# Performance work log

Hardware: AMD Instinct MI355X
Metric: run time of the kernel (lower is better)

Reference implementation:

```python
import jax, jax.numpy as jnp
import numpy as np

DT = 0.1  # integration step used by LiquidCell.forward default

def setup_inputs() -> dict:
    key = jax.random.key(0)
    k1, k2, k3 = jax.random.split(key, 3)
    B, T, I, H = 32, 1024, 512, 1024
    x = jax.random.normal(k1, (B, T, I), dtype=jnp.float32)
    # Linear weights stored torch-style: [out_features, in_features]
    W = jax.random.normal(k2, (H, I), dtype=jnp.float32) * 0.02
    U = jax.random.normal(k3, (H, H), dtype=jnp.float32) * 0.02
    b = jnp.zeros((H,), dtype=jnp.float32)
    tau = jnp.ones((H,), dtype=jnp.float32)
    return {"x": x, "W": W, "U": U, "b": b, "tau": tau}

def reference(x, W, U, b, tau):
    # x: [B, T, I]; returns (h_final [B, H], all_states [B, T, H])
    B = x.shape[0]
    H = tau.shape[0]
    # Precompute input projections for all timesteps in one big GEMM: [B, T, H]
    xW = jnp.einsum('bti,hi->bth', x, W)
    inv_tau = 1.0 / tau

    def step(h, xW_t):
        # xW_t: [B, H]
        act = jnp.tanh(xW_t + h @ U.T + b)
        h_new = h + DT * (-inv_tau * h + act)
        return h_new, h_new

    h0 = jnp.zeros((B, H), dtype=x.dtype)
    xs = jnp.swapaxes(xW, 0, 1)  # [T, B, H]
    h_final, states = jax.lax.scan(step, h0, xs)
    all_states = jnp.swapaxes(states, 0, 1)  # [B, T, H]
    return h_final, all_states
```

## Files before the change

### kernel.cpp

```cpp
#include <hip/hip_runtime.h>


#define DT 0.1f
#define BB 32
#define TT 1024
#define II 512
#define HH 1024

typedef __attribute__((ext_vector_type(4))) float f32x4;
typedef __attribute__((ext_vector_type(8))) short s16x8;

__device__ __forceinline__ unsigned short f2bf(float f) {
  unsigned int u = __builtin_bit_cast(unsigned int, f);
  u += 0x7fffu + ((u >> 16) & 1u);
  return (unsigned short)(u >> 16);
}

__global__ __launch_bounds__(256) void cvt_u_kernel(const float* __restrict__ U,
                                                    unsigned short* __restrict__ Ub) {
  int i4 = (blockIdx.x * 256 + threadIdx.x) * 4;
  float4 v = *(const float4*)(U + i4);
  ushort4 o;
  o.x = f2bf(v.x); o.y = f2bf(v.y); o.z = f2bf(v.z); o.w = f2bf(v.w);
  *(ushort4*)(Ub + i4) = o;
}

#define P1_LDK 36

__global__ __launch_bounds__(256) void xw_gemm(const float* __restrict__ x,
                                               const float* __restrict__ W,
                                               float* __restrict__ out) {
  __shared__ __align__(16) float Xs[128 * P1_LDK];
  __shared__ __align__(16) float Ws_s[128 * P1_LDK];
  const int tid = threadIdx.x;
  const int m0 = blockIdx.y * 128;
  const int n0 = blockIdx.x * 128;
  const int ty = tid >> 4;
  const int tx = tid & 15;
  const int lrow = tid >> 3;
  const int lf = tid & 7;

  float acc[8][8];
#pragma unroll
  for (int i = 0; i < 8; ++i)
#pragma unroll
    for (int j = 0; j < 8; ++j) acc[i][j] = 0.0f;

  for (int kk = 0; kk < II; kk += 32) {
#pragma unroll
    for (int p = 0; p < 4; ++p) {
      int r = lrow + 32 * p;
      float4 vx = *(const float4*)&x[(m0 + r) * II + kk + 4 * lf];
      *(float4*)&Xs[r * P1_LDK + 4 * lf] = vx;
      float4 vw = *(const float4*)&W[(n0 + r) * II + kk + 4 * lf];
      *(float4*)&Ws_s[r * P1_LDK + 4 * lf] = vw;
    }
    __syncthreads();
#pragma unroll
    for (int kq = 0; kq < 32; kq += 4) {
      float4 a[8], b[8];
#pragma unroll
      for (int i = 0; i < 4; ++i) {
        a[i]     = *(const float4*)&Xs[(ty * 4 + i) * P1_LDK + kq];
        a[i + 4] = *(const float4*)&Xs[(ty * 4 + i + 64) * P1_LDK + kq];
      }
#pragma unroll
      for (int j = 0; j < 8; ++j)
        b[j] = *(const float4*)&Ws_s[(tx + 16 * j) * P1_LDK + kq];
#pragma unroll
      for (int i = 0; i < 8; ++i)
#pragma unroll
        for (int j = 0; j < 8; ++j) {
          acc[i][j] += a[i].x * b[j].x;
          acc[i][j] += a[i].y * b[j].y;
          acc[i][j] += a[i].z * b[j].z;
          acc[i][j] += a[i].w * b[j].w;
        }
    }
    __syncthreads();
  }
#pragma unroll
  for (int i = 0; i < 8; ++i) {
    int m = m0 + ty * 4 + (i < 4 ? i : 64 + i - 4);
#pragma unroll
    for (int j = 0; j < 8; ++j)
      out[m * HH + n0 + tx + 16 * j] = acc[i][j];
  }
}

#define LDH 1032

__global__ __launch_bounds__(64) void liquid_step(
    const unsigned short* __restrict__ hb,
    const unsigned short* __restrict__ Ub,
    float* __restrict__ hf,
    unsigned short* __restrict__ hb_out,
    float* __restrict__ states,
    const float* __restrict__ bias,
    const float* __restrict__ tau,
    int t) {
  __shared__ __align__(16) unsigned short h_s[16 * LDH];
  __shared__ __align__(16) unsigned short u_s[8 * LDH];

  const int l = threadIdx.x;
  const int bid = blockIdx.x;
  const int mg = bid >> 7;
  const int jg = bid & 127;
  const int n = l & 15;
  const int q = l >> 4;
  const int jloc = n & 7;
  const int j = jg * 8 + jloc;

  float xw[4], hold[4];
#pragma unroll
  for (int r = 0; r < 4; ++r) {
    int b = mg * 16 + q * 4 + r;
    xw[r] = states[(b * TT + t) * HH + j];
    hold[r] = hf[b * HH + j];
  }
  float bj = bias[j];
  float invt = 1.0f / tau[j];

#pragma unroll
  for (int r = 0; r < 16; ++r) {
    int b = mg * 16 + r;
#pragma unroll
    for (int hh = 0; hh < 2; ++hh) {
      uint4 v = *(const uint4*)(hb + b * HH + hh * 512 + l * 8);
      *(uint4*)&h_s[r * LDH + hh * 512 + l * 8] = v;
    }
  }
#pragma unroll
  for (int r = 0; r < 8; ++r) {
    int jr = jg * 8 + r;
#pragma unroll
    for (int hh = 0; hh < 2; ++hh) {
      uint4 v = *(const uint4*)(Ub + jr * HH + hh * 512 + l * 8);
      *(uint4*)&u_s[r * LDH + hh * 512 + l * 8] = v;
    }
  }
  __syncthreads();

  f32x4 acc0 = {0.f, 0.f, 0.f, 0.f}, acc1 = {0.f, 0.f, 0.f, 0.f};
  const int ar = n;
  const int br = jloc;
  const int ko = q * 8;
#pragma unroll
  for (int kc = 0; kc < 32; kc += 2) {
    s16x8 a0 = *(const s16x8*)&h_s[ar * LDH + kc * 32 + ko];
    s16x8 b0 = *(const s16x8*)&u_s[br * LDH + kc * 32 + ko];
    acc0 = __builtin_amdgcn_mfma_f32_16x16x32_bf16(a0, b0, acc0, 0, 0, 0);
    s16x8 a1 = *(const s16x8*)&h_s[ar * LDH + (kc + 1) * 32 + ko];
    s16x8 b1 = *(const s16x8*)&u_s[br * LDH + (kc + 1) * 32 + ko];
    acc1 = __builtin_amdgcn_mfma_f32_16x16x32_bf16(a1, b1, acc1, 0, 0, 0);
  }
  f32x4 acc = acc0 + acc1;

#pragma unroll
  for (int r = 0; r < 4; ++r) {
    float pre = xw[r] + acc[r] + bj;
    float act = tanhf(pre);
    float hnew = hold[r] + DT * (act - invt * hold[r]);
    if (n < 8) {
      int b = mg * 16 + q * 4 + r;
      hf[b * HH + j] = hnew;
      hb_out[b * HH + j] = f2bf(hnew);
      states[(b * TT + t) * HH + j] = hnew;
    }
  }
}

extern "C" void kernel_launch(void* const* d_in, const int* in_sizes, int n_in,
                              void* d_out, int out_size, void* d_ws, size_t ws_size,
                              hipStream_t stream) {
  const float* x    = (const float*)d_in[0];
  const float* W    = (const float*)d_in[1];
  const float* U    = (const float*)d_in[2];
  const float* bias = (const float*)d_in[3];
  const float* tau  = (const float*)d_in[4];

  float* out = (float*)d_out;
  float* hf = out;
  float* states = out + BB * HH;

  unsigned short* Ub = (unsigned short*)d_ws;
  unsigned short* hb = Ub + (size_t)HH * HH;

  hipMemsetAsync(hf, 0, BB * HH * sizeof(float), stream);
  hipMemsetAsync(hb, 0, BB * HH * sizeof(unsigned short), stream);

  cvt_u_kernel<<<(HH * HH) / (256 * 4), 256, 0, stream>>>(U, Ub);

  xw_gemm<<<dim3(HH / 128, (BB * TT) / 128), 256, 0, stream>>>(x, W, states);

  for (int t = 0; t < TT; ++t) {
    liquid_step<<<256, 64, 0, stream>>>(hb, Ub, hf, hb, states, bias, tau, t);
  }
}
```

Measured before the change: 5.041 ms.

## Replace per-timestep launches with a persistent scan kernel using flag-based sync

Replaces the 1024 separate per-step kernel launches with one persistent kernel of 128 single-wave workgroups. Each workgroup keeps its slice of U in registers and loops over all timesteps. Workgroups in the same batch group synchronise through agent-scope atomic flags, and the bf16 hidden state is double-buffered. This removes per-launch overhead and the repeated reload of U, and it prefetches the next step's xW. It relies on all 128 workgroups being co-resident for the spin-wait to make progress, and it adds polling latency on every step.

```diff
diff --git a/kernel.cpp b/kernel.cpp
--- a/kernel.cpp
+++ b/kernel.cpp
@@ -88,86 +88,94 @@
   }
 }
 
-#define LDH 1032
-
-__global__ __launch_bounds__(64) void liquid_step(
-    const unsigned short* __restrict__ hb,
+__global__ __launch_bounds__(64, 1) void liquid_scan(
     const unsigned short* __restrict__ Ub,
+    unsigned short* __restrict__ hbuf,
+    int* flags,
     float* __restrict__ hf,
-    unsigned short* __restrict__ hb_out,
     float* __restrict__ states,
     const float* __restrict__ bias,
-    const float* __restrict__ tau,
-    int t) {
-  __shared__ __align__(16) unsigned short h_s[16 * LDH];
-  __shared__ __align__(16) unsigned short u_s[8 * LDH];
-
+    const float* __restrict__ tau) {
   const int l = threadIdx.x;
-  const int bid = blockIdx.x;
-  const int mg = bid >> 7;
-  const int jg = bid & 127;
+  const int wg = blockIdx.x;
+  const int mg = wg >> 6;
+  const int jg = wg & 63;
   const int n = l & 15;
   const int q = l >> 4;
-  const int jloc = n & 7;
-  const int j = jg * 8 + jloc;
-
-  float xw[4], hold[4];
-#pragma unroll
-  for (int r = 0; r < 4; ++r) {
-    int b = mg * 16 + q * 4 + r;
-    xw[r] = states[(b * TT + t) * HH + j];
-    hold[r] = hf[b * HH + j];
+  const int j = jg * 16 + n;
+  const int arow = mg * 16 + n;
+
+  s16x8 ufrag[32];
+#pragma unroll
+  for (int kc = 0; kc < 32; ++kc)
+    ufrag[kc] = *(const s16x8*)(Ub + (size_t)j * HH + kc * 32 + q * 8);
+
+  const float bj = bias[j];
+  const float invt = 1.0f / tau[j];
+  int* const myflags = flags + mg * 64;
+
+  float hold[4] = {0.f, 0.f, 0.f, 0.f};
+  float xw[4];
+#pragma unroll
+  for (int r = 0; r < 4; ++r)
+    xw[r] = states[((size_t)(mg * 16 + q * 4 + r) * TT + 0) * HH + j];
+
+  for (int t = 0; t < TT; ++t) {
+    const unsigned short* hin = hbuf + (size_t)(t & 1) * (BB * HH);
+    unsigned short* hout = hbuf + (size_t)((t + 1) & 1) * (BB * HH);
+
+    if (t > 0) {
+      for (;;) {
+        int f = __hip_atomic_load(&myflags[l], __ATOMIC_RELAXED,
+                                  __HIP_MEMORY_SCOPE_AGENT);
+        if (__all(f >= t)) break;
+      }
+      __builtin_amdgcn_fence(__ATOMIC_ACQUIRE, "agent");
+    }
+
+    s16x8 af[32];
+#pragma unroll
+    for (int kc = 0; kc < 32; ++kc)
+      af[kc] = *(const s16x8*)(hin + (size_t)arow * HH + kc * 32 + q * 8);
+
+    const int tn = (t + 1 < TT) ? t + 1 : TT - 1;
+    float xwn[4];
+#pragma unroll
+    for (int r = 0; r < 4; ++r)
+      xwn[r] = states[((size_t)(mg * 16 + q * 4 + r) * TT + tn) * HH + j];
+
+    f32x4 a0 = {0.f, 0.f, 0.f, 0.f}, a1 = {0.f, 0.f, 0.f, 0.f};
+    f32x4 a2 = {0.f, 0.f, 0.f, 0.f}, a3 = {0.f, 0.f, 0.f, 0.f};
+#pragma unroll
+    for (int kc = 0; kc < 32; kc += 4) {
+      a0 = __builtin_amdgcn_mfma_f32_16x16x32_bf16(af[kc + 0], ufrag[kc + 0], a0, 0, 0, 0);
+      a1 = __builtin_amdgcn_mfma_f32_16x16x32_bf16(af[kc + 1], ufrag[kc + 1], a1, 0, 0, 0);
+      a2 = __builtin_amdgcn_mfma_f32_16x16x32_bf16(af[kc + 2], ufrag[kc + 2], a2, 0, 0, 0);
+      a3 = __builtin_amdgcn_mfma_f32_16x16x32_bf16(af[kc + 3], ufrag[kc + 3], a3, 0, 0, 0);
+    }
+    f32x4 acc = (a0 + a1) + (a2 + a3);
+
+#pragma unroll
+    for (int r = 0; r < 4; ++r) {
+      const int b = mg * 16 + q * 4 + r;
+      float pre = xw[r] + acc[r] + bj;
+      float act = tanhf(pre);
+      float hnew = hold[r] + DT * (act - invt * hold[r]);
+      hold[r] = hnew;
+      states[((size_t)b * TT + t) * HH + j] = hnew;
+      hout[b * HH + j] = f2bf(hnew);
+      xw[r] = xwn[r];
+    }
+
+    __builtin_amdgcn_fence(__ATOMIC_RELEASE, "agent");
+    if (l == 0)
+      __hip_atomic_store(&myflags[jg], t + 1, __ATOMIC_RELAXED,
+                         __HIP_MEMORY_SCOPE_AGENT);
   }
-  float bj = bias[j];
-  float invt = 1.0f / tau[j];
-
-#pragma unroll
-  for (int r = 0; r < 16; ++r) {
-    int b = mg * 16 + r;
-#pragma unroll
-    for (int hh = 0; hh < 2; ++hh) {
-      uint4 v = *(const uint4*)(hb + b * HH + hh * 512 + l * 8);
-      *(uint4*)&h_s[r * LDH + hh * 512 + l * 8] = v;
-    }
-  }
-#pragma unroll
-  for (int r = 0; r < 8; ++r) {
-    int jr = jg * 8 + r;
-#pragma unroll
-    for (int hh = 0; hh < 2; ++hh) {
-      uint4 v = *(const uint4*)(Ub + jr * HH + hh * 512 + l * 8);
-      *(uint4*)&u_s[r * LDH + hh * 512 + l * 8] = v;
-    }
-  }
-  __syncthreads();
-
-  f32x4 acc0 = {0.f, 0.f, 0.f, 0.f}, acc1 = {0.f, 0.f, 0.f, 0.f};
-  const int ar = n;
-  const int br = jloc;
-  const int ko = q * 8;
-#pragma unroll
-  for (int kc = 0; kc < 32; kc += 2) {
-    s16x8 a0 = *(const s16x8*)&h_s[ar * LDH + kc * 32 + ko];
-    s16x8 b0 = *(const s16x8*)&u_s[br * LDH + kc * 32 + ko];
-    acc0 = __builtin_amdgcn_mfma_f32_16x16x32_bf16(a0, b0, acc0, 0, 0, 0);
-    s16x8 a1 = *(const s16x8*)&h_s[ar * LDH + (kc + 1) * 32 + ko];
-    s16x8 b1 = *(const s16x8*)&u_s[br * LDH + (kc + 1) * 32 + ko];
-    acc1 = __builtin_amdgcn_mfma_f32_16x16x32_bf16(a1, b1, acc1, 0, 0, 0);
-  }
-  f32x4 acc = acc0 + acc1;
-
-#pragma unroll
-  for (int r = 0; r < 4; ++r) {
-    float pre = xw[r] + acc[r] + bj;
-    float act = tanhf(pre);
-    float hnew = hold[r] + DT * (act - invt * hold[r]);
-    if (n < 8) {
-      int b = mg * 16 + q * 4 + r;
-      hf[b * HH + j] = hnew;
-      hb_out[b * HH + j] = f2bf(hnew);
-      states[(b * TT + t) * HH + j] = hnew;
-    }
-  }
+
+#pragma unroll
+  for (int r = 0; r < 4; ++r)
+    hf[(mg * 16 + q * 4 + r) * HH + j] = hold[r];
 }
 
 extern "C" void kernel_launch(void* const* d_in, const int* in_sizes, int n_in,
@@ -184,16 +192,16 @@
   float* states = out + BB * HH;
 
   unsigned short* Ub = (unsigned short*)d_ws;
-  unsigned short* hb = Ub + (size_t)HH * HH;
-
-  hipMemsetAsync(hf, 0, BB * HH * sizeof(float), stream);
-  hipMemsetAsync(hb, 0, BB * HH * sizeof(unsigned short), stream);
+  unsigned short* hbuf = Ub + (size_t)HH * HH;
+  int* flags = (int*)(hbuf + 2 * BB * HH);
+
+  hipMemsetAsync(hbuf, 0,
+                 2 * BB * HH * sizeof(unsigned short) + 128 * sizeof(int),
+                 stream);
 
   cvt_u_kernel<<<(HH * HH) / (256 * 4), 256, 0, stream>>>(U, Ub);
 
   xw_gemm<<<dim3(HH / 128, (BB * TT) / 128), 256, 0, stream>>>(x, W, states);
 
-  for (int t = 0; t < TT; ++t) {
-    liquid_step<<<256, 64, 0, stream>>>(hb, Ub, hf, hb, states, bias, tau, t);
-  }
-}
+  liquid_scan<<<128, 64, 0, stream>>>(Ub, hbuf, flags, hf, states, bias, tau);
+}
```

New measurement: 9.374 ms. +86.0%, slower.
